# Optimization experiments

Hardware: AMD Instinct MI355X
Metric: run time of the kernel (lower is better)

The kernel has to match this reference:

```python
import jax, jax.numpy as jnp
import numpy as np

TEMPERATURE = 0.07
EPS = 1e-12  # F.normalize default eps

def _l2norm(x):
    n = jnp.linalg.norm(x, axis=1, keepdims=True)
    return x / jnp.maximum(n, EPS)

def setup_inputs() -> dict:
    key = jax.random.key(0)
    k1, k2 = jax.random.split(key)
    N, D = 16384, 256
    return {
        "feat_local": jax.random.normal(k1, (N, D), dtype=jnp.float32),
        "feat_global": jax.random.normal(k2, (N, D), dtype=jnp.float32),
    }

def reference(feat_local, feat_global):
    fl = _l2norm(feat_local)
    fg = _l2norm(feat_global)
    # [N, N] similarity matrix scaled by temperature
    sim = jnp.einsum('nd,md->nm', fl, fg) / TEMPERATURE
    pos_sim = jnp.diagonal(sim)
    loss = -pos_sim + jax.scipy.special.logsumexp(sim, axis=1)
    return loss.mean()
```

## Files before the change

### kernel.cpp

```cpp
#include <hip/hip_runtime.h>
#include <hip/hip_bf16.h>

#define NROWS 16384
#define DIM   256
#define SEGS  8
#define BN    128
#define NT    ((NROWS / SEGS) / BN)
#define INVT  14.285714285714286f
#define C1f   20.60992915555662f
#define LN2f  0.6931471805599453f

typedef __attribute__((ext_vector_type(8)))  int   int8v;
typedef __attribute__((ext_vector_type(16))) float f32x16;

#define SCALE1 0x7F7F7F7F

__global__ __launch_bounds__(256) void norm_diag_kernel(
    const float* __restrict__ fl, const float* __restrict__ fg,
    unsigned char* __restrict__ A, unsigned char* __restrict__ B,
    float* __restrict__ diag, float* __restrict__ out)
{
    int tid  = threadIdx.x;
    int wave = tid >> 6, lane = tid & 63;
    int row  = blockIdx.x * 4 + wave;
    if (blockIdx.x == 0 && tid == 0) out[0] = 0.0f;

    float4 xl = ((const float4*)(fl + (size_t)row * DIM))[lane];
    float4 xg = ((const float4*)(fg + (size_t)row * DIM))[lane];
    float ssl = xl.x*xl.x + xl.y*xl.y + xl.z*xl.z + xl.w*xl.w;
    float ssg = xg.x*xg.x + xg.y*xg.y + xg.z*xg.z + xg.w*xg.w;
    for (int m = 1; m < 64; m <<= 1) {
        ssl += __shfl_xor(ssl, m, 64);
        ssg += __shfl_xor(ssg, m, 64);
    }
    float il = 1.0f / fmaxf(sqrtf(ssl), 1e-12f);
    float ig = 1.0f / fmaxf(sqrtf(ssg), 1e-12f);
    float nl0 = xl.x*il, nl1 = xl.y*il, nl2 = xl.z*il, nl3 = xl.w*il;
    float ng0 = xg.x*ig, ng1 = xg.y*ig, ng2 = xg.z*ig, ng3 = xg.w*ig;

    int pa = __builtin_amdgcn_cvt_pk_fp8_f32(nl0 * C1f, nl1 * C1f, 0, false);
    pa     = __builtin_amdgcn_cvt_pk_fp8_f32(nl2 * C1f, nl3 * C1f, pa, true);
    int pb = __builtin_amdgcn_cvt_pk_fp8_f32(ng0, ng1, 0, false);
    pb     = __builtin_amdgcn_cvt_pk_fp8_f32(ng2, ng3, pb, true);
    ((int*)(A + (size_t)row * DIM))[lane] = pa;

    {
        int kcb = lane >> 2;
        int b4  = lane & 3;
        int c64 = row & 63;
        unsigned chunk = (unsigned)((row >> 7) * 2048 + ((row >> 6) & 1) * 1024
                                    + kcb * 64 + (c64 ^ (kcb & 7)));
        ((int*)B)[chunk * 4 + b4] = pb;
    }

    float d = nl0*ng0 + nl1*ng1 + nl2*ng2 + nl3*ng3;
    for (int m = 1; m < 64; m <<= 1) d += __shfl_xor(d, m, 64);
    if (lane == 0) diag[row] = d;
}

__global__ __launch_bounds__(256, 2) void sim_lse_kernel(
    const unsigned char* __restrict__ A, const unsigned char* __restrict__ B,
    float* __restrict__ lpart)
{
    __shared__ __align__(16) unsigned char bt[2 * BN * DIM];

    int tid  = threadIdx.x;
    int lane = tid & 63;
    int l31  = lane & 31, half = lane >> 5;
    int wave = tid >> 6;
    int rowBase = blockIdx.y * 256 + wave * 64;

    int8v af[2][4];
#pragma unroll
    for (int s = 0; s < 2; ++s) {
        const unsigned char* ap = A + (size_t)(rowBase + s*32 + l31) * DIM + half * 32;
#pragma unroll
        for (int kk = 0; kk < 4; ++kk) {
            int4 lo = *(const int4*)(ap + kk * 64);
            int4 hi = *(const int4*)(ap + kk * 64 + 16);
            int8v v;
            v[0]=lo.x; v[1]=lo.y; v[2]=lo.z; v[3]=lo.w;
            v[4]=hi.x; v[5]=hi.y; v[6]=hi.z; v[7]=hi.w;
            af[s][kk] = v;
        }
    }

    f32x16 lv[2];
    f32x16 Z;
#pragma unroll
    for (int r = 0; r < 16; ++r) { lv[0][r] = 0.0f; lv[1][r] = 0.0f; Z[r] = 0.0f; }

    int T0 = blockIdx.x * NT;

    auto stage = [&](int T, unsigned bufo) {
        const unsigned char* g = B + (size_t)T * (BN * DIM) + (wave * 512 + lane) * 16;
        unsigned lo = bufo + (unsigned)(wave * 512) * 16;
#pragma unroll
        for (int j = 0; j < 8; ++j) {
            __builtin_amdgcn_global_load_lds(
                (const __attribute__((address_space(1))) unsigned int*)(g + j * 1024),
                (__attribute__((address_space(3))) unsigned int*)&bt[lo + j * 1024],
                16, 0, 0);
        }
    };

    stage(T0, 0);

    for (int t = 0; t < NT; ++t) {
        unsigned bufo = (t & 1) ? (unsigned)(BN * DIM) : 0u;
        __syncthreads();

        if (t + 1 < NT)
            stage(T0 + t + 1, (t & 1) ? 0u : (unsigned)(BN * DIM));

#pragma unroll
        for (int p = 0; p < 2; ++p) {
            unsigned subo = bufo + (unsigned)p * 16384;
            f32x16 acc[2][2];
#pragma unroll
            for (int kk = 0; kk < 4; ++kk) {
                int8v bfr[2];
#pragma unroll
                for (int c = 0; c < 2; ++c) {
                    int col = c * 32 + l31;
                    int kcb = kk * 4 + half * 2;
                    unsigned p0 = (unsigned)(kcb * 64 + (col ^ (kcb & 7)));
                    unsigned p1 = (unsigned)((kcb + 1) * 64 + (col ^ ((kcb + 1) & 7)));
                    int4 lo = *(const int4*)&bt[subo + p0 * 16];
                    int4 hi = *(const int4*)&bt[subo + p1 * 16];
                    int8v v;
                    v[0]=lo.x; v[1]=lo.y; v[2]=lo.z; v[3]=lo.w;
                    v[4]=hi.x; v[5]=hi.y; v[6]=hi.z; v[7]=hi.w;
                    bfr[c] = v;
                }
#pragma unroll
                for (int c = 0; c < 2; ++c) {
                    if (kk == 0) {
                        acc[0][c] = __builtin_amdgcn_mfma_scale_f32_32x32x64_f8f6f4(
                            af[0][0], bfr[c], Z, 0, 0, 0, SCALE1, 0, SCALE1);
                        acc[1][c] = __builtin_amdgcn_mfma_scale_f32_32x32x64_f8f6f4(
                            af[1][0], bfr[c], Z, 0, 0, 0, SCALE1, 0, SCALE1);
                    } else {
                        acc[0][c] = __builtin_amdgcn_mfma_scale_f32_32x32x64_f8f6f4(
                            af[0][kk], bfr[c], acc[0][c], 0, 0, 0, SCALE1, 0, SCALE1);
                        acc[1][c] = __builtin_amdgcn_mfma_scale_f32_32x32x64_f8f6f4(
                            af[1][kk], bfr[c], acc[1][c], 0, 0, 0, SCALE1, 0, SCALE1);
                    }
                }
            }
#pragma unroll
            for (int s = 0; s < 2; ++s) {
                f32x16 e;
#pragma unroll
                for (int r = 0; r < 16; ++r)
                    e[r] = __builtin_amdgcn_exp2f(acc[s][0][r]) + __builtin_amdgcn_exp2f(acc[s][1][r]);
                lv[s] += e;
            }
        }
    }

#pragma unroll
    for (int s = 0; s < 2; ++s)
#pragma unroll
        for (int r = 0; r < 16; ++r) {
            float v = lv[s][r];
            v += __shfl_xor(v, 1, 64);
            v += __shfl_xor(v, 2, 64);
            v += __shfl_xor(v, 4, 64);
            v += __shfl_xor(v, 8, 64);
            v += __shfl_xor(v, 16, 64);
            lv[s][r] = v;
        }
    if (l31 == 0) {
#pragma unroll
        for (int s = 0; s < 2; ++s)
#pragma unroll
            for (int r = 0; r < 16; ++r) {
                int row = rowBase + s*32 + (r & 3) + 8*(r >> 2) + 4*half;
                lpart[(size_t)blockIdx.x * NROWS + row] = lv[s][r];
            }
    }
}

__global__ __launch_bounds__(256) void reduce_kernel(
    const float* __restrict__ lpart, const float* __restrict__ diag,
    float* __restrict__ out)
{
    __shared__ float sm[4];
    int gtid = blockIdx.x * 256 + threadIdx.x;
    float s = 0.0f;
    for (int row = gtid; row < NROWS; row += 32 * 256) {
        float t = 0.0f;
#pragma unroll
        for (int g = 0; g < SEGS; ++g) t += lpart[(size_t)g * NROWS + row];
        s += LN2f * log2f(t) - INVT * diag[row];
    }
    for (int m = 1; m < 64; m <<= 1) s += __shfl_xor(s, m, 64);
    int wave = threadIdx.x >> 6, lane = threadIdx.x & 63;
    if (lane == 0) sm[wave] = s;
    __syncthreads();
    if (threadIdx.x == 0) {
        float tot = sm[0] + sm[1] + sm[2] + sm[3];
        atomicAdd(out, tot * (1.0f / NROWS));
    }
}

extern "C" void kernel_launch(void* const* d_in, const int* in_sizes, int n_in,
                              void* d_out, int out_size, void* d_ws, size_t ws_size,
                              hipStream_t stream) {
    const float* fl = (const float*)d_in[0];
    const float* fg = (const float*)d_in[1];
    float* out = (float*)d_out;

    char* ws = (char*)d_ws;
    unsigned char* A = (unsigned char*)ws;
    unsigned char* B = A + (size_t)NROWS * DIM;
    float* diag  = (float*)(ws + 2 * (size_t)NROWS * DIM);
    float* lpart = diag + NROWS;

    norm_diag_kernel<<<NROWS / 4, 256, 0, stream>>>(fl, fg, A, B, diag, out);
    sim_lse_kernel<<<dim3(SEGS, NROWS / 256), 256, 0, stream>>>(A, B, lpart);
    reduce_kernel<<<32, 256, 0, stream>>>(lpart, diag, out);
}
```

Baseline: 141.6 us.

## Software-pipeline exp epilogue with MFMA and fold final reduction into last block

The exp2 epilogue for one 64-column sub-tile is deferred so it runs while the MFMAs of the next sub-tile are issued, aiming to overlap transcendental work with matrix math. The separate reduce kernel is removed: a global atomic counter picks the last finishing block, which does the log-sum and mean itself. This saves a kernel launch but keeps two accumulator sets live, which raises register pressure, and leaves a serial single-block reduction at the tail.

```diff
diff --git a/kernel.cpp b/kernel.cpp
--- a/kernel.cpp
+++ b/kernel.cpp
@@ -6,6 +6,7 @@
 #define SEGS  8
 #define BN    128
 #define NT    ((NROWS / SEGS) / BN)
+#define NBLK  (SEGS * (NROWS / 256))
 #define INVT  14.285714285714286f
 #define C1f   20.60992915555662f
 #define LN2f  0.6931471805599453f
@@ -18,12 +19,12 @@
 __global__ __launch_bounds__(256) void norm_diag_kernel(
     const float* __restrict__ fl, const float* __restrict__ fg,
     unsigned char* __restrict__ A, unsigned char* __restrict__ B,
-    float* __restrict__ diag, float* __restrict__ out)
+    float* __restrict__ diag, unsigned* __restrict__ cnt)
 {
     int tid  = threadIdx.x;
     int wave = tid >> 6, lane = tid & 63;
     int row  = blockIdx.x * 4 + wave;
-    if (blockIdx.x == 0 && tid == 0) out[0] = 0.0f;
+    if (blockIdx.x == 0 && tid == 0) cnt[0] = 0;
 
     float4 xl = ((const float4*)(fl + (size_t)row * DIM))[lane];
     float4 xg = ((const float4*)(fg + (size_t)row * DIM))[lane];
@@ -60,7 +61,8 @@
 
 __global__ __launch_bounds__(256, 2) void sim_lse_kernel(
     const unsigned char* __restrict__ A, const unsigned char* __restrict__ B,
-    float* __restrict__ lpart)
+    float* __restrict__ lpart, const float* __restrict__ diag,
+    unsigned* __restrict__ cnt, float* __restrict__ out)
 {
     __shared__ __align__(16) unsigned char bt[2 * BN * DIM];
 
@@ -68,6 +70,7 @@
     int lane = tid & 63;
     int l31  = lane & 31, half = lane >> 5;
     int wave = tid >> 6;
+    int seg  = blockIdx.x;
     int rowBase = blockIdx.y * 256 + wave * 64;
 
     int8v af[2][4];
@@ -90,7 +93,7 @@
 #pragma unroll
     for (int r = 0; r < 16; ++r) { lv[0][r] = 0.0f; lv[1][r] = 0.0f; Z[r] = 0.0f; }
 
-    int T0 = blockIdx.x * NT;
+    int T0 = seg * NT;
 
     auto stage = [&](int T, unsigned bufo) {
         const unsigned char* g = B + (size_t)T * (BN * DIM) + (wave * 512 + lane) * 16;
@@ -104,7 +107,20 @@
         }
     };
 
+    auto epi = [&](f32x16 (&ac)[2][2]) {
+#pragma unroll
+        for (int s = 0; s < 2; ++s) {
+            f32x16 e;
+#pragma unroll
+            for (int r = 0; r < 16; ++r)
+                e[r] = __builtin_amdgcn_exp2f(ac[s][0][r]) + __builtin_amdgcn_exp2f(ac[s][1][r]);
+            lv[s] += e;
+        }
+    };
+
     stage(T0, 0);
+
+    f32x16 accP[2][2][2];
 
     for (int t = 0; t < NT; ++t) {
         unsigned bufo = (t & 1) ? (unsigned)(BN * DIM) : 0u;
@@ -116,7 +132,7 @@
 #pragma unroll
         for (int p = 0; p < 2; ++p) {
             unsigned subo = bufo + (unsigned)p * 16384;
-            f32x16 acc[2][2];
+            f32x16 (&acc)[2][2] = accP[p];
 #pragma unroll
             for (int kk = 0; kk < 4; ++kk) {
                 int8v bfr[2];
@@ -148,16 +164,11 @@
                     }
                 }
             }
-#pragma unroll
-            for (int s = 0; s < 2; ++s) {
-                f32x16 e;
-#pragma unroll
-                for (int r = 0; r < 16; ++r)
-                    e[r] = __builtin_amdgcn_exp2f(acc[s][0][r]) + __builtin_amdgcn_exp2f(acc[s][1][r]);
-                lv[s] += e;
-            }
-        }
-    }
+            if (p == 0) { if (t > 0) epi(accP[1]); }
+            else         epi(accP[0]);
+        }
+    }
+    epi(accP[1]);
 
 #pragma unroll
     for (int s = 0; s < 2; ++s)
@@ -177,31 +188,29 @@
 #pragma unroll
             for (int r = 0; r < 16; ++r) {
                 int row = rowBase + s*32 + (r & 3) + 8*(r >> 2) + 4*half;
-                lpart[(size_t)blockIdx.x * NROWS + row] = lv[s][r];
+                lpart[(size_t)seg * NROWS + row] = lv[s][r];
             }
     }
-}
-
-__global__ __launch_bounds__(256) void reduce_kernel(
-    const float* __restrict__ lpart, const float* __restrict__ diag,
-    float* __restrict__ out)
-{
-    __shared__ float sm[4];
-    int gtid = blockIdx.x * 256 + threadIdx.x;
-    float s = 0.0f;
-    for (int row = gtid; row < NROWS; row += 32 * 256) {
-        float t = 0.0f;
-#pragma unroll
-        for (int g = 0; g < SEGS; ++g) t += lpart[(size_t)g * NROWS + row];
-        s += LN2f * log2f(t) - INVT * diag[row];
-    }
-    for (int m = 1; m < 64; m <<= 1) s += __shfl_xor(s, m, 64);
-    int wave = threadIdx.x >> 6, lane = threadIdx.x & 63;
-    if (lane == 0) sm[wave] = s;
+
+    __threadfence();
+    __shared__ unsigned lastdone;
+    if (tid == 0) lastdone = (atomicAdd(cnt, 1u) == (unsigned)(NBLK - 1));
     __syncthreads();
-    if (threadIdx.x == 0) {
-        float tot = sm[0] + sm[1] + sm[2] + sm[3];
-        atomicAdd(out, tot * (1.0f / NROWS));
+    if (lastdone) {
+        __threadfence();
+        float s = 0.0f;
+        for (int row = tid; row < NROWS; row += 256) {
+            float tt = 0.0f;
+#pragma unroll
+            for (int g = 0; g < SEGS; ++g) tt += lpart[(size_t)g * NROWS + row];
+            s += LN2f * log2f(tt) - INVT * diag[row];
+        }
+        for (int m = 1; m < 64; m <<= 1) s += __shfl_xor(s, m, 64);
+        float* sm = (float*)bt;
+        if ((tid & 63) == 0) sm[tid >> 6] = s;
+        __syncthreads();
+        if (tid == 0)
+            out[0] = (sm[0] + sm[1] + sm[2] + sm[3]) * (1.0f / NROWS);
     }
 }
 
@@ -217,8 +226,8 @@
     unsigned char* B = A + (size_t)NROWS * DIM;
     float* diag  = (float*)(ws + 2 * (size_t)NROWS * DIM);
     float* lpart = diag + NROWS;
-
-    norm_diag_kernel<<<NROWS / 4, 256, 0, stream>>>(fl, fg, A, B, diag, out);
-    sim_lse_kernel<<<dim3(SEGS, NROWS / 256), 256, 0, stream>>>(A, B, lpart);
-    reduce_kernel<<<32, 256, 0, stream>>>(lpart, diag, out);
+    unsigned* cnt = (unsigned*)(lpart + (size_t)SEGS * NROWS);
+
+    norm_diag_kernel<<<NROWS / 4, 256, 0, stream>>>(fl, fg, A, B, diag, cnt);
+    sim_lse_kernel<<<dim3(SEGS, NROWS / 256), 256, 0, stream>>>(A, B, lpart, diag, cnt, out);
 }
```

Result: slower. 267.1 us (+88.7%).

## Software-pipeline MFMA chains with exp epilogue using double accumulators

Applied to the files above, without the earlier changes.

Splits each subtile's matrix-multiply work into two column chains with separate accumulator sets. The exp2 epilogue of one chain is interleaved with the MFMA chain of the other, so transcendental VALU work can overlap matrix-core work. The running sums start at -1 to cancel the priming epilogue on zero accumulators, and a final epilogue drains the last chain. This needs extra accumulator registers, which could hurt occupancy or cause spills.

```diff
diff --git a/kernel.cpp b/kernel.cpp
--- a/kernel.cpp
+++ b/kernel.cpp
@@ -68,6 +68,7 @@
     int lane = tid & 63;
     int l31  = lane & 31, half = lane >> 5;
     int wave = tid >> 6;
+    int seg  = blockIdx.x;
     int rowBase = blockIdx.y * 256 + wave * 64;
 
     int8v af[2][4];
@@ -87,10 +88,15 @@
 
     f32x16 lv[2];
     f32x16 Z;
-#pragma unroll
-    for (int r = 0; r < 16; ++r) { lv[0][r] = 0.0f; lv[1][r] = 0.0f; Z[r] = 0.0f; }
-
-    int T0 = blockIdx.x * NT;
+    f32x16 accA[2], accB[2];
+#pragma unroll
+    for (int r = 0; r < 16; ++r) {
+        lv[0][r] = -1.0f; lv[1][r] = -1.0f;
+        Z[r] = 0.0f;
+        accB[0][r] = 0.0f; accB[1][r] = 0.0f;
+    }
+
+    int T0 = seg * NT;
 
     auto stage = [&](int T, unsigned bufo) {
         const unsigned char* g = B + (size_t)T * (BN * DIM) + (wave * 512 + lane) * 16;
@@ -104,6 +110,45 @@
         }
     };
 
+    auto chain = [&](f32x16 (&ac)[2], int c, unsigned subo) {
+        int8v bfr[4];
+#pragma unroll
+        for (int kk = 0; kk < 4; ++kk) {
+            int col = c * 32 + l31;
+            int kcb = kk * 4 + half * 2;
+            unsigned p0 = (unsigned)(kcb * 64 + (col ^ (kcb & 7)));
+            unsigned p1 = (unsigned)((kcb + 1) * 64 + (col ^ ((kcb + 1) & 7)));
+            int4 lo = *(const int4*)&bt[subo + p0 * 16];
+            int4 hi = *(const int4*)&bt[subo + p1 * 16];
+            int8v v;
+            v[0]=lo.x; v[1]=lo.y; v[2]=lo.z; v[3]=lo.w;
+            v[4]=hi.x; v[5]=hi.y; v[6]=hi.z; v[7]=hi.w;
+            bfr[kk] = v;
+        }
+        ac[0] = __builtin_amdgcn_mfma_scale_f32_32x32x64_f8f6f4(
+            af[0][0], bfr[0], Z, 0, 0, 0, SCALE1, 0, SCALE1);
+        ac[1] = __builtin_amdgcn_mfma_scale_f32_32x32x64_f8f6f4(
+            af[1][0], bfr[0], Z, 0, 0, 0, SCALE1, 0, SCALE1);
+#pragma unroll
+        for (int kk = 1; kk < 4; ++kk) {
+            ac[0] = __builtin_amdgcn_mfma_scale_f32_32x32x64_f8f6f4(
+                af[0][kk], bfr[kk], ac[0], 0, 0, 0, SCALE1, 0, SCALE1);
+            ac[1] = __builtin_amdgcn_mfma_scale_f32_32x32x64_f8f6f4(
+                af[1][kk], bfr[kk], ac[1], 0, 0, 0, SCALE1, 0, SCALE1);
+        }
+    };
+
+    auto epi = [&](f32x16 (&ac)[2]) {
+#pragma unroll
+        for (int s = 0; s < 2; ++s) {
+            f32x16 e;
+#pragma unroll
+            for (int r = 0; r < 16; ++r)
+                e[r] = __builtin_amdgcn_exp2f(ac[s][r]);
+            lv[s] += e;
+        }
+    };
+
     stage(T0, 0);
 
     for (int t = 0; t < NT; ++t) {
@@ -116,48 +161,13 @@
 #pragma unroll
         for (int p = 0; p < 2; ++p) {
             unsigned subo = bufo + (unsigned)p * 16384;
-            f32x16 acc[2][2];
-#pragma unroll
-            for (int kk = 0; kk < 4; ++kk) {
-                int8v bfr[2];
-#pragma unroll
-                for (int c = 0; c < 2; ++c) {
-                    int col = c * 32 + l31;
-                    int kcb = kk * 4 + half * 2;
-                    unsigned p0 = (unsigned)(kcb * 64 + (col ^ (kcb & 7)));
-                    unsigned p1 = (unsigned)((kcb + 1) * 64 + (col ^ ((kcb + 1) & 7)));
-                    int4 lo = *(const int4*)&bt[subo + p0 * 16];
-                    int4 hi = *(const int4*)&bt[subo + p1 * 16];
-                    int8v v;
-                    v[0]=lo.x; v[1]=lo.y; v[2]=lo.z; v[3]=lo.w;
-                    v[4]=hi.x; v[5]=hi.y; v[6]=hi.z; v[7]=hi.w;
-                    bfr[c] = v;
-                }
-#pragma unroll
-                for (int c = 0; c < 2; ++c) {
-                    if (kk == 0) {
-                        acc[0][c] = __builtin_amdgcn_mfma_scale_f32_32x32x64_f8f6f4(
-                            af[0][0], bfr[c], Z, 0, 0, 0, SCALE1, 0, SCALE1);
-                        acc[1][c] = __builtin_amdgcn_mfma_scale_f32_32x32x64_f8f6f4(
-                            af[1][0], bfr[c], Z, 0, 0, 0, SCALE1, 0, SCALE1);
-                    } else {
-                        acc[0][c] = __builtin_amdgcn_mfma_scale_f32_32x32x64_f8f6f4(
-                            af[0][kk], bfr[c], acc[0][c], 0, 0, 0, SCALE1, 0, SCALE1);
-                        acc[1][c] = __builtin_amdgcn_mfma_scale_f32_32x32x64_f8f6f4(
-                            af[1][kk], bfr[c], acc[1][c], 0, 0, 0, SCALE1, 0, SCALE1);
-                    }
-                }
-            }
-#pragma unroll
-            for (int s = 0; s < 2; ++s) {
-                f32x16 e;
-#pragma unroll
-                for (int r = 0; r < 16; ++r)
-                    e[r] = __builtin_amdgcn_exp2f(acc[s][0][r]) + __builtin_amdgcn_exp2f(acc[s][1][r]);
-                lv[s] += e;
-            }
-        }
-    }
+            chain(accA, 0, subo);
+            epi(accB);
+            chain(accB, 1, subo);
+            epi(accA);
+        }
+    }
+    epi(accB);
 
 #pragma unroll
     for (int s = 0; s < 2; ++s)
@@ -177,7 +187,7 @@
 #pragma unroll
             for (int r = 0; r < 16; ++r) {
                 int row = rowBase + s*32 + (r & 3) + 8*(r >> 2) + 4*half;
-                lpart[(size_t)blockIdx.x * NROWS + row] = lv[s][r];
+                lpart[(size_t)seg * NROWS + row] = lv[s][r];
             }
     }
 }
```

Measured after the change: 139.2 us. Within noise of the previous version (-1.7%).
